# Kernel optimization log

Hardware: AMD Instinct MI355X
Metric: run time of the kernel (lower is better)

## Reference

```python
import jax, jax.numpy as jnp
import numpy as np

FILTER_K = 100  # filter_K from __init__
NUM_CLASSES = 1000


def setup_inputs() -> dict:
    key = jax.random.key(0)
    ks = jax.random.split(key, 7)
    B, Din, D, C, N = 256, 2048, 512, NUM_CLASSES, 50000
    x = jax.random.normal(ks[0], (B, Din), jnp.float32)
    Wf = jax.random.normal(ks[1], (Din, D), jnp.float32) * 0.02
    Wc = jax.random.normal(ks[2], (C, D), jnp.float32) * 0.05
    bc = jax.random.normal(ks[3], (C,), jnp.float32) * 0.01
    supports_in = jax.random.normal(ks[4], (N, D), jnp.float32)
    ent_in = jax.random.uniform(ks[5], (N,), jnp.float32)
    labels_idx = jax.random.randint(ks[6], (N,), 0, C)
    return {"x": x, "Wf": Wf, "Wc": Wc, "bc": bc,
            "supports_in": supports_in, "ent_in": ent_in, "labels_idx": labels_idx}


def _softmax_entropy(logits):
    # -(softmax * log_softmax).sum(1), computed stably in one pass
    logp = jax.nn.log_softmax(logits, axis=1)
    return -(jnp.exp(logp) * logp).sum(axis=1)


def reference(x, Wf, Wc, bc, supports_in, ent_in, labels_idx):
    C = Wc.shape[0]
    z = x @ Wf                    # featurizer: [B, D]
    p = z @ Wc.T + bc             # classifier logits: [B, C]
    yhat = jax.nn.one_hot(jnp.argmax(p, axis=1), C, dtype=z.dtype)
    ent_new = _softmax_entropy(p)
    labels_in = jax.nn.one_hot(labels_idx, C, dtype=z.dtype)

    # grow support memory
    supports = jnp.concatenate([supports_in, z], axis=0)   # [M, D]
    labels = jnp.concatenate([labels_in, yhat], axis=0)    # [M, C]
    ent = jnp.concatenate([ent_in, ent_new], axis=0)       # [M]

    # select_supports: per-class keep FILTER_K lowest-entropy entries.
    # Torch gathers a variable-size subset; equivalent fixed-shape form is a
    # boolean mask (non-selected rows contribute zero to the weights matmul).
    y = jnp.argmax(labels, axis=1)
    M = ent.shape[0]
    order = jnp.lexsort((ent, y))            # sort by class, then entropy
    y_sorted = y[order]
    # rank of each entry within its class segment
    rank = jnp.arange(M) - jnp.searchsorted(y_sorted, y_sorted, side='left')
    mask = jnp.zeros((M,), bool).at[order].set(rank < FILTER_K)
    maskf = mask.astype(z.dtype)

    # normalize supports row-wise (F.normalize, eps=1e-12), then masked matmul
    s_norm = supports / jnp.maximum(
        jnp.linalg.norm(supports, axis=1, keepdims=True), 1e-12)
    weights = (s_norm * maskf[:, None]).T @ (labels * maskf[:, None])  # [D, C]
    weights = weights / jnp.maximum(
        jnp.linalg.norm(weights, axis=0, keepdims=True), 1e-12)
    return z @ weights            # [B, C]
```

## Files before the change

kernel.cpp:

```cpp
#include <hip/hip_runtime.h>
#include <hip/hip_bf16.h>
#include <math.h>

#define BB   256
#define DIN  2048
#define DD   512
#define CC   1000
#define NN   50000
#define MM   (NN + BB)
#define FILTER_K 100
#define SLOT 512

#define SK1  16
#define SK2  8

#define Z_OFF     0
#define CNT_OFF   (Z_OFF + BB*DD)
#define ENTN_OFF  (CNT_OFF + 1024)
#define CLS_OFF   (ENTN_OFF + BB)
#define ENTS_OFF  (CLS_OFF + BB)
#define IDXS_OFF  (ENTS_OFF + CC*SLOT)
#define WN_OFF    (IDXS_OFF + CC*SLOT)
#define ZP_OFF    (WN_OFF + CC*DD)
#define PP_OFF    (ZP_OFF + SK1*BB*DD)
#define OP_OFF    (PP_OFF + SK2*BB*CC)

#define BM 64
#define BN 128
#define BK 16

__global__ __launch_bounds__(256, 2) void gemm_ab_part(
    const float* __restrict__ A, const float* __restrict__ B,
    float* __restrict__ Cp, int M, int N, int K, int klen) {
  __shared__ float As[BK][BM + 4];
  __shared__ float Bs[BK][BN + 4];
  const int tid = threadIdx.x;
  const int m0 = blockIdx.y * BM;
  const int n0 = blockIdx.x * BN;
  const int k0 = blockIdx.z * klen;
  const int ar = tid >> 2, ac = (tid & 3) * 4;
  const int br = tid >> 4, bc = (tid & 15) * 8;
  const int tm = (tid >> 4) * 4;
  const int tn = (tid & 15) * 4;
  float acc[4][8] = {};
  for (int kk = 0; kk < klen; kk += BK) {
    float4 av  = *(const float4*)&A[(size_t)(m0 + ar) * K + (k0 + kk + ac)];
    float4 bv0 = *(const float4*)&B[(size_t)(k0 + kk + br) * N + (n0 + bc)];
    float4 bv1 = *(const float4*)&B[(size_t)(k0 + kk + br) * N + (n0 + bc + 4)];
    __syncthreads();
    As[ac + 0][ar] = av.x; As[ac + 1][ar] = av.y;
    As[ac + 2][ar] = av.z; As[ac + 3][ar] = av.w;
    *(float4*)&Bs[br][bc] = bv0;
    *(float4*)&Bs[br][bc + 4] = bv1;
    __syncthreads();
#pragma unroll
    for (int q = 0; q < BK; ++q) {
      float4 a  = *(const float4*)&As[q][tm];
      float4 b0 = *(const float4*)&Bs[q][tn];
      float4 b1 = *(const float4*)&Bs[q][tn + 64];
      float aa[4] = {a.x, a.y, a.z, a.w};
      float bb[8] = {b0.x, b0.y, b0.z, b0.w, b1.x, b1.y, b1.z, b1.w};
#pragma unroll
      for (int i = 0; i < 4; ++i)
#pragma unroll
        for (int j = 0; j < 8; ++j) acc[i][j] += aa[i] * bb[j];
    }
  }
  float* Cb = Cp + (size_t)blockIdx.z * M * N;
#pragma unroll
  for (int i = 0; i < 4; ++i) {
    *(float4*)&Cb[(size_t)(m0 + tm + i) * N + (n0 + tn)] =
        make_float4(acc[i][0], acc[i][1], acc[i][2], acc[i][3]);
    *(float4*)&Cb[(size_t)(m0 + tm + i) * N + (n0 + 64 + tn)] =
        make_float4(acc[i][4], acc[i][5], acc[i][6], acc[i][7]);
  }
}

__global__ __launch_bounds__(256, 2) void gemm_abt_part(
    const float* __restrict__ A, const float* __restrict__ B,
    float* __restrict__ Cp, int M, int L, int K, int klen) {
  __shared__ float As[BK][BM + 4];
  __shared__ float Bs[BK][BN + 4];
  const int tid = threadIdx.x;
  const int m0 = blockIdx.y * BM;
  const int n0 = blockIdx.x * BN;
  const int k0 = blockIdx.z * klen;
  const int ar = tid >> 2, ac = (tid & 3) * 4;
  const int br = tid >> 2, bc = (tid & 3) * 4;
  const int tm = (tid >> 4) * 4;
  const int tn = (tid & 15) * 4;
  float acc[4][8] = {};
  for (int kk = 0; kk < klen; kk += BK) {
    float4 av = *(const float4*)&A[(size_t)(m0 + ar) * K + (k0 + kk + ac)];
    float4 bv0 = make_float4(0.f, 0.f, 0.f, 0.f);
    float4 bv1 = make_float4(0.f, 0.f, 0.f, 0.f);
    if (n0 + br < L)
      bv0 = *(const float4*)&B[(size_t)(n0 + br) * K + (k0 + kk + bc)];
    if (n0 + 64 + br < L)
      bv1 = *(const float4*)&B[(size_t)(n0 + 64 + br) * K + (k0 + kk + bc)];
    __syncthreads();
    As[ac + 0][ar] = av.x; As[ac + 1][ar] = av.y;
    As[ac + 2][ar] = av.z; As[ac + 3][ar] = av.w;
    Bs[bc + 0][br] = bv0.x; Bs[bc + 1][br] = bv0.y;
    Bs[bc + 2][br] = bv0.z; Bs[bc + 3][br] = bv0.w;
    Bs[bc + 0][br + 64] = bv1.x; Bs[bc + 1][br + 64] = bv1.y;
    Bs[bc + 2][br + 64] = bv1.z; Bs[bc + 3][br + 64] = bv1.w;
    __syncthreads();
#pragma unroll
    for (int q = 0; q < BK; ++q) {
      float4 a  = *(const float4*)&As[q][tm];
      float4 b0 = *(const float4*)&Bs[q][tn];
      float4 b1 = *(const float4*)&Bs[q][tn + 64];
      float aa[4] = {a.x, a.y, a.z, a.w};
      float bb[8] = {b0.x, b0.y, b0.z, b0.w, b1.x, b1.y, b1.z, b1.w};
#pragma unroll
      for (int i = 0; i < 4; ++i)
#pragma unroll
        for (int j = 0; j < 8; ++j) acc[i][j] += aa[i] * bb[j];
    }
  }
  float* Cb = Cp + (size_t)blockIdx.z * M * L;
#pragma unroll
  for (int i = 0; i < 4; ++i)
#pragma unroll
    for (int j = 0; j < 4; ++j) {
      int n = n0 + tn + j;
      if (n < L) Cb[(size_t)(m0 + tm + i) * L + n] = acc[i][j];
      int n2 = n0 + 64 + tn + j;
      if (n2 < L) Cb[(size_t)(m0 + tm + i) * L + n2] = acc[i][j + 4];
    }
}

template <int S>
__global__ __launch_bounds__(256) void reduce_part(
    const float* __restrict__ part, float* __restrict__ out, int n4) {
  int i = blockIdx.x * 256 + threadIdx.x;
  if (i >= n4) return;
  const float4* p4 = (const float4*)part;
  float4 a = p4[i];
#pragma unroll
  for (int s = 1; s < S; ++s) {
    float4 b = p4[(size_t)s * n4 + i];
    a.x += b.x; a.y += b.y; a.z += b.z; a.w += b.w;
  }
  ((float4*)out)[i] = a;
}

__global__ __launch_bounds__(256) void rowstats(
    const float* __restrict__ ppart, const float* __restrict__ bc,
    float* __restrict__ ent_new, int* __restrict__ cls) {
  const int b = blockIdx.x, tid = threadIdx.x;
  const int lane = tid & 63, wid = tid >> 6;
  float r[4];
  float mv = -INFINITY; int mi = 0x7fffffff;
#pragma unroll
  for (int i = 0; i < 4; ++i) {
    int c = tid + 256 * i;
    if (c < CC) {
      float v = bc[c];
#pragma unroll
      for (int s = 0; s < SK2; ++s)
        v += ppart[(size_t)s * BB * CC + (size_t)b * CC + c];
      r[i] = v;
    } else {
      r[i] = -INFINITY;
    }
    if (r[i] > mv) { mv = r[i]; mi = c; }
  }
#pragma unroll
  for (int o = 32; o > 0; o >>= 1) {
    float ov = __shfl_down(mv, o, 64);
    int oi = __shfl_down(mi, o, 64);
    if (ov > mv || (ov == mv && oi < mi)) { mv = ov; mi = oi; }
  }
  __shared__ float smv[4]; __shared__ int smi[4];
  if (lane == 0) { smv[wid] = mv; smi[wid] = mi; }
  __syncthreads();
  if (tid == 0) {
#pragma unroll
    for (int w = 1; w < 4; ++w)
      if (smv[w] > smv[0] || (smv[w] == smv[0] && smi[w] < smi[0])) {
        smv[0] = smv[w]; smi[0] = smi[w];
      }
  }
  __syncthreads();
  const float m = smv[0]; const int am = smi[0];
  float s = 0.f, t = 0.f;
#pragma unroll
  for (int i = 0; i < 4; ++i) {
    if (tid + 256 * i < CC) {
      float u = r[i] - m;
      float e = expf(u);
      s += e; t += u * e;
    }
  }
#pragma unroll
  for (int o = 32; o > 0; o >>= 1) {
    s += __shfl_down(s, o, 64);
    t += __shfl_down(t, o, 64);
  }
  __shared__ float ssum[4], tsum[4];
  if (lane == 0) { ssum[wid] = s; tsum[wid] = t; }
  __syncthreads();
  if (tid == 0) {
    float S = ssum[0] + ssum[1] + ssum[2] + ssum[3];
    float T = tsum[0] + tsum[1] + tsum[2] + tsum[3];
    ent_new[b] = logf(S) - T / S;
    cls[b] = am;
  }
}

__global__ void scatter(const int* __restrict__ labels_idx,
                        const int* __restrict__ cls,
                        const float* __restrict__ ent_in,
                        const float* __restrict__ ent_new,
                        int* __restrict__ cnt,
                        float* __restrict__ ent_s, int* __restrict__ idx_s) {
  int m = blockIdx.x * blockDim.x + threadIdx.x;
  if (m >= MM) return;
  int c; float e;
  if (m < NN) { c = labels_idx[m]; e = ent_in[m]; }
  else        { c = cls[m - NN];   e = ent_new[m - NN]; }
  int pos = atomicAdd(&cnt[c], 1);
  if (pos < SLOT) {
    ent_s[(size_t)c * SLOT + pos] = e;
    idx_s[(size_t)c * SLOT + pos] = m;
  }
}

__global__ __launch_bounds__(256) void class_weights(
    const float* __restrict__ supports_in, const float* __restrict__ z,
    const float* __restrict__ ent_s, const int* __restrict__ idx_s,
    const int* __restrict__ cnt, float* __restrict__ wn) {
  const int c = blockIdx.x, tid = threadIdx.x;
  const int lane = tid & 63, wid = tid >> 6;
  int n = cnt[c]; if (n > SLOT) n = SLOT;

  __shared__ int sel[SLOT];
  __shared__ float se[SLOT];
  __shared__ int si[SLOT];
  int seln;
  if (n <= FILTER_K) {
    seln = n;
    for (int i = tid; i < n; i += 256) sel[i] = idx_s[(size_t)c * SLOT + i];
  } else {
    for (int i = tid; i < SLOT; i += 256) {
      if (i < n) { se[i] = ent_s[(size_t)c * SLOT + i]; si[i] = idx_s[(size_t)c * SLOT + i]; }
      else       { se[i] = INFINITY;                     si[i] = 0x7fffffff; }
    }
    __syncthreads();
    for (int k = 2; k <= SLOT; k <<= 1)
      for (int j = k >> 1; j > 0; j >>= 1) {
        for (int i = tid; i < SLOT; i += 256) {
          int ixj = i ^ j;
          if (ixj > i) {
            bool up = ((i & k) == 0);
            float e1 = se[i], e2 = se[ixj];
            int i1 = si[i], i2 = si[ixj];
            bool gt = (e1 > e2) || (e1 == e2 && i1 > i2);
            if (gt == up) { se[i] = e2; se[ixj] = e1; si[i] = i2; si[ixj] = i1; }
          }
        }
        __syncthreads();
      }
    seln = FILTER_K;
    for (int i = tid; i < FILTER_K; i += 256) sel[i] = si[i];
  }
  __syncthreads();

  float4 a0 = make_float4(0.f, 0.f, 0.f, 0.f), a1 = a0;
  for (int j = wid; j < seln; j += 4) {
    int ridx = sel[j];
    const float4* p4 = (const float4*)((ridx < NN)
        ? supports_in + (size_t)ridx * DD
        : z + (size_t)(ridx - NN) * DD);
    float4 v0 = p4[lane * 2], v1 = p4[lane * 2 + 1];
    float s = v0.x * v0.x + v0.y * v0.y + v0.z * v0.z + v0.w * v0.w
            + v1.x * v1.x + v1.y * v1.y + v1.z * v1.z + v1.w * v1.w;
#pragma unroll
    for (int o = 1; o < 64; o <<= 1) s += __shfl_xor(s, o, 64);
    float sc = 1.0f / fmaxf(sqrtf(s), 1e-12f);
    a0.x += v0.x * sc; a0.y += v0.y * sc; a0.z += v0.z * sc; a0.w += v0.w * sc;
    a1.x += v1.x * sc; a1.y += v1.y * sc; a1.z += v1.z * sc; a1.w += v1.w * sc;
  }

  __shared__ float part[4][DD];
  *(float4*)&part[wid][lane * 8] = a0;
  *(float4*)&part[wid][lane * 8 + 4] = a1;
  __syncthreads();
  const int d = tid * 2;
  float2 w;
  w.x = part[0][d] + part[1][d] + part[2][d] + part[3][d];
  w.y = part[0][d + 1] + part[1][d + 1] + part[2][d + 1] + part[3][d + 1];
  float ss = w.x * w.x + w.y * w.y;
#pragma unroll
  for (int o = 1; o < 64; o <<= 1) ss += __shfl_xor(ss, o, 64);
  __shared__ float tot[4];
  if (lane == 0) tot[wid] = ss;
  __syncthreads();
  float S = tot[0] + tot[1] + tot[2] + tot[3];
  float sc = 1.0f / fmaxf(sqrtf(S), 1e-12f);
  ((float2*)(wn + (size_t)c * DD))[tid] = make_float2(w.x * sc, w.y * sc);
}

extern "C" void kernel_launch(void* const* d_in, const int* in_sizes, int n_in,
                              void* d_out, int out_size, void* d_ws, size_t ws_size,
                              hipStream_t stream) {
  (void)in_sizes; (void)n_in; (void)out_size; (void)ws_size;
  const float* x           = (const float*)d_in[0];
  const float* Wf          = (const float*)d_in[1];
  const float* Wc          = (const float*)d_in[2];
  const float* bc          = (const float*)d_in[3];
  const float* supports_in = (const float*)d_in[4];
  const float* ent_in      = (const float*)d_in[5];
  const int*   labels_idx  = (const int*)d_in[6];
  float* out = (float*)d_out;

  float* W = (float*)d_ws;
  float* z       = W + Z_OFF;
  int*   cnt     = (int*)(W + CNT_OFF);
  float* ent_new = W + ENTN_OFF;
  int*   cls     = (int*)(W + CLS_OFF);
  float* ent_s   = W + ENTS_OFF;
  int*   idx_s   = (int*)(W + IDXS_OFF);
  float* wn      = W + WN_OFF;
  float* zpart   = W + ZP_OFF;
  float* ppart   = W + PP_OFF;
  float* opart   = W + OP_OFF;

  hipMemsetAsync(cnt, 0, 1024 * sizeof(int), stream);

  gemm_ab_part<<<dim3(DD / BN, BB / BM, SK1), 256, 0, stream>>>(
      x, Wf, zpart, BB, DD, DIN, DIN / SK1);
  reduce_part<SK1><<<(BB * DD / 4 + 255) / 256, 256, 0, stream>>>(
      zpart, z, BB * DD / 4);

  gemm_abt_part<<<dim3((CC + BN - 1) / BN, BB / BM, SK2), 256, 0, stream>>>(
      z, Wc, ppart, BB, CC, DD, DD / SK2);
  rowstats<<<BB, 256, 0, stream>>>(ppart, bc, ent_new, cls);

  scatter<<<(MM + 255) / 256, 256, 0, stream>>>(
      labels_idx, cls, ent_in, ent_new, cnt, ent_s, idx_s);
  class_weights<<<CC, 256, 0, stream>>>(supports_in, z, ent_s, idx_s, cnt, wn);

  gemm_abt_part<<<dim3((CC + BN - 1) / BN, BB / BM, SK2), 256, 0, stream>>>(
      z, wn, opart, BB, CC, DD, DD / SK2);
  reduce_part<SK2><<<(BB * CC / 4 + 255) / 256, 256, 0, stream>>>(
      opart, out, BB * CC / 4);
}
```

Before: 238.6 us.

## Prefetch GEMM tiles, shrink ABT tiles, fold scatter into rowstats, pair row loads

Several changes land together. The two split-K GEMMs now prefetch the next k-tile into registers while the current tile is computed, and use fixed compile-time sizes. The featurizer GEMM moves to a k-split of 32 and the transposed GEMMs to 64x64 tiles with float4 stores. The support scatter runs before the GEMMs, and the new-sample scatter is fused into rowstats so a separate kernel launch is removed. class_weights loads two support rows per iteration to raise memory-level parallelism. The cost is more partial buffers to reduce and smaller tiles with less reuse per block.

```diff
diff --git a/kernel.cpp b/kernel.cpp
--- a/kernel.cpp
+++ b/kernel.cpp
@@ -11,50 +11,48 @@
 #define FILTER_K 100
 #define SLOT 512
 
-#define SK1  16
-#define SK2  8
+#define SK1  32
+#define SKP  8
 
 #define Z_OFF     0
 #define CNT_OFF   (Z_OFF + BB*DD)
-#define ENTN_OFF  (CNT_OFF + 1024)
-#define CLS_OFF   (ENTN_OFF + BB)
-#define ENTS_OFF  (CLS_OFF + BB)
+#define ENTS_OFF  (CNT_OFF + 1024)
 #define IDXS_OFF  (ENTS_OFF + CC*SLOT)
 #define WN_OFF    (IDXS_OFF + CC*SLOT)
 #define ZP_OFF    (WN_OFF + CC*DD)
 #define PP_OFF    (ZP_OFF + SK1*BB*DD)
-#define OP_OFF    (PP_OFF + SK2*BB*CC)
-
-#define BM 64
-#define BN 128
-#define BK 16
+#define OP_OFF    (PP_OFF + SKP*BB*CC)
 
 __global__ __launch_bounds__(256, 2) void gemm_ab_part(
     const float* __restrict__ A, const float* __restrict__ B,
-    float* __restrict__ Cp, int M, int N, int K, int klen) {
-  __shared__ float As[BK][BM + 4];
-  __shared__ float Bs[BK][BN + 4];
+    float* __restrict__ Cp) {
+  __shared__ float As[16][68];
+  __shared__ float Bs[16][132];
   const int tid = threadIdx.x;
-  const int m0 = blockIdx.y * BM;
-  const int n0 = blockIdx.x * BN;
-  const int k0 = blockIdx.z * klen;
+  const int m0 = blockIdx.y * 64;
+  const int n0 = blockIdx.x * 128;
+  const int k0 = blockIdx.z * 64;
   const int ar = tid >> 2, ac = (tid & 3) * 4;
-  const int br = tid >> 4, bc = (tid & 15) * 8;
-  const int tm = (tid >> 4) * 4;
-  const int tn = (tid & 15) * 4;
+  const int br = tid >> 4, bcn = (tid & 15) * 8;
+  const int tm = (tid >> 4) * 4, tn = (tid & 15) * 4;
   float acc[4][8] = {};
-  for (int kk = 0; kk < klen; kk += BK) {
-    float4 av  = *(const float4*)&A[(size_t)(m0 + ar) * K + (k0 + kk + ac)];
-    float4 bv0 = *(const float4*)&B[(size_t)(k0 + kk + br) * N + (n0 + bc)];
-    float4 bv1 = *(const float4*)&B[(size_t)(k0 + kk + br) * N + (n0 + bc + 4)];
+  float4 av  = *(const float4*)&A[(size_t)(m0 + ar) * DIN + k0 + ac];
+  float4 bv0 = *(const float4*)&B[(size_t)(k0 + br) * DD + n0 + bcn];
+  float4 bv1 = *(const float4*)&B[(size_t)(k0 + br) * DD + n0 + bcn + 4];
+  for (int kk = 0; kk < 64; kk += 16) {
     __syncthreads();
     As[ac + 0][ar] = av.x; As[ac + 1][ar] = av.y;
     As[ac + 2][ar] = av.z; As[ac + 3][ar] = av.w;
-    *(float4*)&Bs[br][bc] = bv0;
-    *(float4*)&Bs[br][bc + 4] = bv1;
-    __syncthreads();
-#pragma unroll
-    for (int q = 0; q < BK; ++q) {
+    *(float4*)&Bs[br][bcn] = bv0;
+    *(float4*)&Bs[br][bcn + 4] = bv1;
+    __syncthreads();
+    if (kk + 16 < 64) {
+      av  = *(const float4*)&A[(size_t)(m0 + ar) * DIN + k0 + kk + 16 + ac];
+      bv0 = *(const float4*)&B[(size_t)(k0 + kk + 16 + br) * DD + n0 + bcn];
+      bv1 = *(const float4*)&B[(size_t)(k0 + kk + 16 + br) * DD + n0 + bcn + 4];
+    }
+#pragma unroll
+    for (int q = 0; q < 16; ++q) {
       float4 a  = *(const float4*)&As[q][tm];
       float4 b0 = *(const float4*)&Bs[q][tn];
       float4 b1 = *(const float4*)&Bs[q][tn + 64];
@@ -66,69 +64,68 @@
         for (int j = 0; j < 8; ++j) acc[i][j] += aa[i] * bb[j];
     }
   }
-  float* Cb = Cp + (size_t)blockIdx.z * M * N;
+  float* Cb = Cp + (size_t)blockIdx.z * BB * DD;
 #pragma unroll
   for (int i = 0; i < 4; ++i) {
-    *(float4*)&Cb[(size_t)(m0 + tm + i) * N + (n0 + tn)] =
+    *(float4*)&Cb[(size_t)(m0 + tm + i) * DD + n0 + tn] =
         make_float4(acc[i][0], acc[i][1], acc[i][2], acc[i][3]);
-    *(float4*)&Cb[(size_t)(m0 + tm + i) * N + (n0 + 64 + tn)] =
+    *(float4*)&Cb[(size_t)(m0 + tm + i) * DD + n0 + 64 + tn] =
         make_float4(acc[i][4], acc[i][5], acc[i][6], acc[i][7]);
   }
 }
 
 __global__ __launch_bounds__(256, 2) void gemm_abt_part(
-    const float* __restrict__ A, const float* __restrict__ B,
-    float* __restrict__ Cp, int M, int L, int K, int klen) {
-  __shared__ float As[BK][BM + 4];
-  __shared__ float Bs[BK][BN + 4];
+    const float* __restrict__ A, const float* __restrict__ Bm,
+    float* __restrict__ Cp) {
+  __shared__ float As[16][68];
+  __shared__ float Bs[16][68];
   const int tid = threadIdx.x;
-  const int m0 = blockIdx.y * BM;
-  const int n0 = blockIdx.x * BN;
-  const int k0 = blockIdx.z * klen;
+  const int m0 = blockIdx.y * 64;
+  const int n0 = blockIdx.x * 64;
+  const int k0 = blockIdx.z * 64;
   const int ar = tid >> 2, ac = (tid & 3) * 4;
-  const int br = tid >> 2, bc = (tid & 3) * 4;
-  const int tm = (tid >> 4) * 4;
-  const int tn = (tid & 15) * 4;
-  float acc[4][8] = {};
-  for (int kk = 0; kk < klen; kk += BK) {
-    float4 av = *(const float4*)&A[(size_t)(m0 + ar) * K + (k0 + kk + ac)];
-    float4 bv0 = make_float4(0.f, 0.f, 0.f, 0.f);
-    float4 bv1 = make_float4(0.f, 0.f, 0.f, 0.f);
-    if (n0 + br < L)
-      bv0 = *(const float4*)&B[(size_t)(n0 + br) * K + (k0 + kk + bc)];
-    if (n0 + 64 + br < L)
-      bv1 = *(const float4*)&B[(size_t)(n0 + 64 + br) * K + (k0 + kk + bc)];
+  const int tm = (tid >> 4) * 4, tn = (tid & 15) * 4;
+  float acc[4][4] = {};
+  float4 av = *(const float4*)&A[(size_t)(m0 + ar) * DD + k0 + ac];
+  float4 bv = make_float4(0.f, 0.f, 0.f, 0.f);
+  if (n0 + ar < CC) bv = *(const float4*)&Bm[(size_t)(n0 + ar) * DD + k0 + ac];
+  for (int kk = 0; kk < 64; kk += 16) {
     __syncthreads();
     As[ac + 0][ar] = av.x; As[ac + 1][ar] = av.y;
     As[ac + 2][ar] = av.z; As[ac + 3][ar] = av.w;
-    Bs[bc + 0][br] = bv0.x; Bs[bc + 1][br] = bv0.y;
-    Bs[bc + 2][br] = bv0.z; Bs[bc + 3][br] = bv0.w;
-    Bs[bc + 0][br + 64] = bv1.x; Bs[bc + 1][br + 64] = bv1.y;
-    Bs[bc + 2][br + 64] = bv1.z; Bs[bc + 3][br + 64] = bv1.w;
-    __syncthreads();
-#pragma unroll
-    for (int q = 0; q < BK; ++q) {
-      float4 a  = *(const float4*)&As[q][tm];
-      float4 b0 = *(const float4*)&Bs[q][tn];
-      float4 b1 = *(const float4*)&Bs[q][tn + 64];
+    Bs[ac + 0][ar] = bv.x; Bs[ac + 1][ar] = bv.y;
+    Bs[ac + 2][ar] = bv.z; Bs[ac + 3][ar] = bv.w;
+    __syncthreads();
+    if (kk + 16 < 64) {
+      av = *(const float4*)&A[(size_t)(m0 + ar) * DD + k0 + kk + 16 + ac];
+      if (n0 + ar < CC)
+        bv = *(const float4*)&Bm[(size_t)(n0 + ar) * DD + k0 + kk + 16 + ac];
+    }
+#pragma unroll
+    for (int q = 0; q < 16; ++q) {
+      float4 a = *(const float4*)&As[q][tm];
+      float4 b = *(const float4*)&Bs[q][tn];
       float aa[4] = {a.x, a.y, a.z, a.w};
-      float bb[8] = {b0.x, b0.y, b0.z, b0.w, b1.x, b1.y, b1.z, b1.w};
+      float bb[4] = {b.x, b.y, b.z, b.w};
 #pragma unroll
       for (int i = 0; i < 4; ++i)
 #pragma unroll
-        for (int j = 0; j < 8; ++j) acc[i][j] += aa[i] * bb[j];
-    }
-  }
-  float* Cb = Cp + (size_t)blockIdx.z * M * L;
-#pragma unroll
-  for (int i = 0; i < 4; ++i)
-#pragma unroll
-    for (int j = 0; j < 4; ++j) {
-      int n = n0 + tn + j;
-      if (n < L) Cb[(size_t)(m0 + tm + i) * L + n] = acc[i][j];
-      int n2 = n0 + 64 + tn + j;
-      if (n2 < L) Cb[(size_t)(m0 + tm + i) * L + n2] = acc[i][j + 4];
-    }
+        for (int j = 0; j < 4; ++j) acc[i][j] += aa[i] * bb[j];
+    }
+  }
+  float* Cb = Cp + (size_t)blockIdx.z * BB * CC;
+#pragma unroll
+  for (int i = 0; i < 4; ++i) {
+    int n = n0 + tn;
+    if (n + 3 < CC) {
+      *(float4*)&Cb[(size_t)(m0 + tm + i) * CC + n] =
+          make_float4(acc[i][0], acc[i][1], acc[i][2], acc[i][3]);
+    } else {
+#pragma unroll
+      for (int j = 0; j < 4; ++j)
+        if (n + j < CC) Cb[(size_t)(m0 + tm + i) * CC + n + j] = acc[i][j];
+    }
+  }
 }
 
 template <int S>
@@ -146,9 +143,24 @@
   ((float4*)out)[i] = a;
 }
 
+__global__ void scatter_old(const int* __restrict__ labels_idx,
+                            const float* __restrict__ ent_in,
+                            int* __restrict__ cnt,
+                            float* __restrict__ ent_s, int* __restrict__ idx_s) {
+  int m = blockIdx.x * blockDim.x + threadIdx.x;
+  if (m >= NN) return;
+  int c = labels_idx[m];
+  int pos = atomicAdd(&cnt[c], 1);
+  if (pos < SLOT) {
+    ent_s[(size_t)c * SLOT + pos] = ent_in[m];
+    idx_s[(size_t)c * SLOT + pos] = m;
+  }
+}
+
 __global__ __launch_bounds__(256) void rowstats(
     const float* __restrict__ ppart, const float* __restrict__ bc,
-    float* __restrict__ ent_new, int* __restrict__ cls) {
+    int* __restrict__ cnt, float* __restrict__ ent_s,
+    int* __restrict__ idx_s) {
   const int b = blockIdx.x, tid = threadIdx.x;
   const int lane = tid & 63, wid = tid >> 6;
   float r[4];
@@ -159,12 +171,10 @@
     if (c < CC) {
       float v = bc[c];
 #pragma unroll
-      for (int s = 0; s < SK2; ++s)
+      for (int s = 0; s < SKP; ++s)
         v += ppart[(size_t)s * BB * CC + (size_t)b * CC + c];
       r[i] = v;
-    } else {
-      r[i] = -INFINITY;
-    }
+    } else r[i] = -INFINITY;
     if (r[i] > mv) { mv = r[i]; mi = c; }
   }
 #pragma unroll
@@ -174,6 +184,7 @@
     if (ov > mv || (ov == mv && oi < mi)) { mv = ov; mi = oi; }
   }
   __shared__ float smv[4]; __shared__ int smi[4];
+  __shared__ float ssm[4], tsm[4];
   if (lane == 0) { smv[wid] = mv; smi[wid] = mi; }
   __syncthreads();
   if (tid == 0) {
@@ -199,32 +210,17 @@
     s += __shfl_down(s, o, 64);
     t += __shfl_down(t, o, 64);
   }
-  __shared__ float ssum[4], tsum[4];
-  if (lane == 0) { ssum[wid] = s; tsum[wid] = t; }
+  if (lane == 0) { ssm[wid] = s; tsm[wid] = t; }
   __syncthreads();
   if (tid == 0) {
-    float S = ssum[0] + ssum[1] + ssum[2] + ssum[3];
-    float T = tsum[0] + tsum[1] + tsum[2] + tsum[3];
-    ent_new[b] = logf(S) - T / S;
-    cls[b] = am;
-  }
-}
-
-__global__ void scatter(const int* __restrict__ labels_idx,
-                        const int* __restrict__ cls,
-                        const float* __restrict__ ent_in,
-                        const float* __restrict__ ent_new,
-                        int* __restrict__ cnt,
-                        float* __restrict__ ent_s, int* __restrict__ idx_s) {
-  int m = blockIdx.x * blockDim.x + threadIdx.x;
-  if (m >= MM) return;
-  int c; float e;
-  if (m < NN) { c = labels_idx[m]; e = ent_in[m]; }
-  else        { c = cls[m - NN];   e = ent_new[m - NN]; }
-  int pos = atomicAdd(&cnt[c], 1);
-  if (pos < SLOT) {
-    ent_s[(size_t)c * SLOT + pos] = e;
-    idx_s[(size_t)c * SLOT + pos] = m;
+    float S = ssm[0] + ssm[1] + ssm[2] + ssm[3];
+    float T = tsm[0] + tsm[1] + tsm[2] + tsm[3];
+    float ent = logf(S) - T / S;
+    int pos = atomicAdd(&cnt[am], 1);
+    if (pos < SLOT) {
+      ent_s[(size_t)am * SLOT + pos] = ent;
+      idx_s[(size_t)am * SLOT + pos] = NN + b;
+    }
   }
 }
 
@@ -269,19 +265,43 @@
   __syncthreads();
 
   float4 a0 = make_float4(0.f, 0.f, 0.f, 0.f), a1 = a0;
-  for (int j = wid; j < seln; j += 4) {
-    int ridx = sel[j];
-    const float4* p4 = (const float4*)((ridx < NN)
-        ? supports_in + (size_t)ridx * DD
-        : z + (size_t)(ridx - NN) * DD);
-    float4 v0 = p4[lane * 2], v1 = p4[lane * 2 + 1];
-    float s = v0.x * v0.x + v0.y * v0.y + v0.z * v0.z + v0.w * v0.w
-            + v1.x * v1.x + v1.y * v1.y + v1.z * v1.z + v1.w * v1.w;
-#pragma unroll
-    for (int o = 1; o < 64; o <<= 1) s += __shfl_xor(s, o, 64);
-    float sc = 1.0f / fmaxf(sqrtf(s), 1e-12f);
-    a0.x += v0.x * sc; a0.y += v0.y * sc; a0.z += v0.z * sc; a0.w += v0.w * sc;
-    a1.x += v1.x * sc; a1.y += v1.y * sc; a1.z += v1.z * sc; a1.w += v1.w * sc;
+  const int npair = seln >> 1;
+  for (int t = wid; t < npair; t += 4) {
+    int r0 = sel[2 * t], r1 = sel[2 * t + 1];
+    const float4* p0 = (const float4*)((r0 < NN)
+        ? supports_in + (size_t)r0 * DD : z + (size_t)(r0 - NN) * DD);
+    const float4* p1 = (const float4*)((r1 < NN)
+        ? supports_in + (size_t)r1 * DD : z + (size_t)(r1 - NN) * DD);
+    float4 u0 = p0[lane * 2], u1 = p0[lane * 2 + 1];
+    float4 w0 = p1[lane * 2], w1 = p1[lane * 2 + 1];
+    float s0 = u0.x * u0.x + u0.y * u0.y + u0.z * u0.z + u0.w * u0.w
+             + u1.x * u1.x + u1.y * u1.y + u1.z * u1.z + u1.w * u1.w;
+    float s1 = w0.x * w0.x + w0.y * w0.y + w0.z * w0.z + w0.w * w0.w
+             + w1.x * w1.x + w1.y * w1.y + w1.z * w1.z + w1.w * w1.w;
+#pragma unroll
+    for (int o = 1; o < 64; o <<= 1) {
+      s0 += __shfl_xor(s0, o, 64);
+      s1 += __shfl_xor(s1, o, 64);
+    }
+    float c0 = 1.0f / fmaxf(sqrtf(s0), 1e-12f);
+    float c1 = 1.0f / fmaxf(sqrtf(s1), 1e-12f);
+    a0.x += u0.x * c0 + w0.x * c1; a0.y += u0.y * c0 + w0.y * c1;
+    a0.z += u0.z * c0 + w0.z * c1; a0.w += u0.w * c0 + w0.w * c1;
+    a1.x += u1.x * c0 + w1.x * c1; a1.y += u1.y * c0 + w1.y * c1;
+    a1.z += u1.z * c0 + w1.z * c1; a1.w += u1.w * c0 + w1.w * c1;
+  }
+  if ((seln & 1) && wid == (npair & 3)) {
+    int r0 = sel[seln - 1];
+    const float4* p0 = (const float4*)((r0 < NN)
+        ? supports_in + (size_t)r0 * DD : z + (size_t)(r0 - NN) * DD);
+    float4 u0 = p0[lane * 2], u1 = p0[lane * 2 + 1];
+    float s0 = u0.x * u0.x + u0.y * u0.y + u0.z * u0.z + u0.w * u0.w
+             + u1.x * u1.x + u1.y * u1.y + u1.z * u1.z + u1.w * u1.w;
+#pragma unroll
+    for (int o = 1; o < 64; o <<= 1) s0 += __shfl_xor(s0, o, 64);
+    float c0 = 1.0f / fmaxf(sqrtf(s0), 1e-12f);
+    a0.x += u0.x * c0; a0.y += u0.y * c0; a0.z += u0.z * c0; a0.w += u0.w * c0;
+    a1.x += u1.x * c0; a1.y += u1.y * c0; a1.z += u1.z * c0; a1.w += u1.w * c0;
   }
 
   __shared__ float part[4][DD];
@@ -289,10 +309,9 @@
   *(float4*)&part[wid][lane * 8 + 4] = a1;
   __syncthreads();
   const int d = tid * 2;
-  float2 w;
-  w.x = part[0][d] + part[1][d] + part[2][d] + part[3][d];
-  w.y = part[0][d + 1] + part[1][d + 1] + part[2][d + 1] + part[3][d + 1];
-  float ss = w.x * w.x + w.y * w.y;
+  float wx = part[0][d] + part[1][d] + part[2][d] + part[3][d];
+  float wy = part[0][d + 1] + part[1][d + 1] + part[2][d + 1] + part[3][d + 1];
+  float ss = wx * wx + wy * wy;
 #pragma unroll
   for (int o = 1; o < 64; o <<= 1) ss += __shfl_xor(ss, o, 64);
   __shared__ float tot[4];
@@ -300,7 +319,7 @@
   __syncthreads();
   float S = tot[0] + tot[1] + tot[2] + tot[3];
   float sc = 1.0f / fmaxf(sqrtf(S), 1e-12f);
-  ((float2*)(wn + (size_t)c * DD))[tid] = make_float2(w.x * sc, w.y * sc);
+  ((float2*)(wn + (size_t)c * DD))[tid] = make_float2(wx * sc, wy * sc);
 }
 
 extern "C" void kernel_launch(void* const* d_in, const int* in_sizes, int n_in,
@@ -317,34 +336,32 @@
   float* out = (float*)d_out;
 
   float* W = (float*)d_ws;
-  float* z       = W + Z_OFF;
-  int*   cnt     = (int*)(W + CNT_OFF);
-  float* ent_new = W + ENTN_OFF;
-  int*   cls     = (int*)(W + CLS_OFF);
-  float* ent_s   = W + ENTS_OFF;
-  int*   idx_s   = (int*)(W + IDXS_OFF);
-  float* wn      = W + WN_OFF;
-  float* zpart   = W + ZP_OFF;
-  float* ppart   = W + PP_OFF;
-  float* opart   = W + OP_OFF;
+  float* z     = W + Z_OFF;
+  int*   cnt   = (int*)(W + CNT_OFF);
+  float* ent_s = W + ENTS_OFF;
+  int*   idx_s = (int*)(W + IDXS_OFF);
+  float* wn    = W + WN_OFF;
+  float* zpart = W + ZP_OFF;
+  float* ppart = W + PP_OFF;
+  float* opart = W + OP_OFF;
 
   hipMemsetAsync(cnt, 0, 1024 * sizeof(int), stream);
 
-  gemm_ab_part<<<dim3(DD / BN, BB / BM, SK1), 256, 0, stream>>>(
-      x, Wf, zpart, BB, DD, DIN, DIN / SK1);
+  scatter_old<<<(NN + 255) / 256, 256, 0, stream>>>(
+      labels_idx, ent_in, cnt, ent_s, idx_s);
+
+  gemm_ab_part<<<dim3(DD / 128, BB / 64, SK1), 256, 0, stream>>>(x, Wf, zpart);
   reduce_part<SK1><<<(BB * DD / 4 + 255) / 256, 256, 0, stream>>>(
       zpart, z, BB * DD / 4);
 
-  gemm_abt_part<<<dim3((CC + BN - 1) / BN, BB / BM, SK2), 256, 0, stream>>>(
-      z, Wc, ppart, BB, CC, DD, DD / SK2);
-  rowstats<<<BB, 256, 0, stream>>>(ppart, bc, ent_new, cls);
-
-  scatter<<<(MM + 255) / 256, 256, 0, stream>>>(
-      labels_idx, cls, ent_in, ent_new, cnt, ent_s, idx_s);
+  gemm_abt_part<<<dim3((CC + 63) / 64, BB / 64, SKP), 256, 0, stream>>>(
+      z, Wc, ppart);
+  rowstats<<<BB, 256, 0, stream>>>(ppart, bc, cnt, ent_s, idx_s);
+
   class_weights<<<CC, 256, 0, stream>>>(supports_in, z, ent_s, idx_s, cnt, wn);
 
-  gemm_abt_part<<<dim3((CC + BN - 1) / BN, BB / BM, SK2), 256, 0, stream>>>(
-      z, wn, opart, BB, CC, DD, DD / SK2);
-  reduce_part<SK2><<<(BB * CC / 4 + 255) / 256, 256, 0, stream>>>(
+  gemm_abt_part<<<dim3((CC + 63) / 64, BB / 64, SKP), 256, 0, stream>>>(
+      z, wn, opart);
+  reduce_part<SKP><<<(BB * CC / 4 + 255) / 256, 256, 0, stream>>>(
       opart, out, BB * CC / 4);
 }
```

Result: faster. 225.9 us (-5.3%).
